# Performance work log

Measured on AMD Instinct MI355X. Metric: run time of the kernel, lower is better.

Reference implementation:

```python
import jax, jax.numpy as jnp
import numpy as np

N_ENT = 40943
N_REL = 237
RANK = 500
BATCH = 1024
NBR = 5
INPUT_SIZE = 600  # neighbor_length(5) * prod(range(1,6)) = 5*120
INIT = 0.001
MIN_NORM = 1e-15
BALL_EPS = 4e-3  # float32 ball projection eps (standard in AttH/GIE repos)


def _artanh(x):
    x = jnp.clip(x, -1.0 + 1e-5, 1.0 - 1e-5)
    return 0.5 * (jnp.log1p(x) - jnp.log1p(-x))


def _project(x, c):
    norm = jnp.maximum(jnp.linalg.norm(x, axis=-1, keepdims=True), MIN_NORM)
    maxnorm = (1.0 - BALL_EPS) / jnp.sqrt(c)
    return jnp.where(norm > maxnorm, x / norm * maxnorm, x)


def _expmap0(u, c):
    sqrt_c = jnp.sqrt(c)
    u_norm = jnp.maximum(jnp.linalg.norm(u, axis=-1, keepdims=True), MIN_NORM)
    gamma = jnp.tanh(sqrt_c * u_norm) * u / (sqrt_c * u_norm)
    return _project(gamma, c)


def _logmap0(y, c):
    sqrt_c = jnp.sqrt(c)
    y_norm = jnp.maximum(jnp.linalg.norm(y, axis=-1, keepdims=True), MIN_NORM)
    return y / y_norm / sqrt_c * _artanh(sqrt_c * y_norm)


def _givens_rotations(r, x):
    b = r.shape[0]
    g = r.reshape(b, -1, 2)
    g = g / jnp.maximum(jnp.linalg.norm(g, axis=-1, keepdims=True), MIN_NORM)
    xr = x.reshape(b, -1, 2)
    x_rot = g[..., 0:1] * xr + g[..., 1:2] * jnp.concatenate([-xr[..., 1:2], xr[..., 0:1]], axis=-1)
    return x_rot.reshape(b, -1)


def setup_inputs() -> dict:
    key = jax.random.key(0)
    ks = jax.random.split(key, 24)
    x = jnp.stack([
        jax.random.randint(ks[0], (BATCH,), 0, N_ENT),
        jax.random.randint(ks[1], (BATCH,), 0, N_REL),
        jax.random.randint(ks[2], (BATCH,), 0, N_ENT),
    ], axis=1)
    neighbors = jnp.concatenate([
        jax.random.randint(ks[3], (N_ENT, NBR, 1), 0, N_ENT),      # neighbor entity ids
        jax.random.randint(ks[4], (N_ENT, NBR, 1), 0, N_REL + 1),  # neighbor rel ids (incl. pad)
    ], axis=2)
    position = jax.random.normal(ks[5], (N_ENT, INPUT_SIZE), jnp.float32)
    lim1 = 1.0 / np.sqrt(INPUT_SIZE)
    lim2 = 1.0 / np.sqrt(RANK)
    limm = 1.0 / np.sqrt(N_REL)
    return {
        'x': x,
        'neighbors': neighbors,
        'position': position,
        'emb_e': INIT * jax.random.normal(ks[6], (N_ENT, 2 * RANK), jnp.float32),
        'emb_r': INIT * jax.random.normal(ks[7], (N_REL + 1, 2 * RANK), jnp.float32),
        'emb1_r': INIT * jax.random.normal(ks[8], (N_REL + 1, 2 * RANK), jnp.float32),
        'context_vec': INIT * jax.random.normal(ks[9], (N_REL, RANK), jnp.float32),
        'neighbor_vec_w': INIT * jax.random.normal(ks[10], (N_REL + 1, RANK), jnp.float32),
        'position_vec_w': INIT * jax.random.normal(ks[11], (N_ENT, INPUT_SIZE), jnp.float32),
        'c1_p': jnp.ones((N_REL, 1), jnp.float32),
        'c2_p': jnp.ones((N_REL, 1), jnp.float32),
        'ab_p': jnp.ones((N_REL + 1, 1), jnp.float32),
        'fc1_w': jax.random.uniform(ks[12], (RANK, INPUT_SIZE), jnp.float32, -lim1, lim1),
        'fc1_b': jax.random.uniform(ks[13], (RANK,), jnp.float32, -lim1, lim1),
        'fc2_w': jax.random.uniform(ks[14], (RANK, RANK), jnp.float32, -lim2, lim2),
        'fc2_b': jax.random.uniform(ks[15], (RANK,), jnp.float32, -lim2, lim2),
        'fc3_w': jax.random.uniform(ks[16], (RANK, RANK), jnp.float32, -lim2, lim2),
        'fc3_b': jax.random.uniform(ks[17], (RANK,), jnp.float32, -lim2, lim2),
        'ln_g': jnp.ones((RANK,), jnp.float32),
        'ln_b': jnp.zeros((RANK,), jnp.float32),
        'fc_mn_w': jax.random.uniform(ks[18], (1, N_REL), jnp.float32, -limm, limm),
        'fc_mn_b': jax.random.uniform(ks[19], (1,), jnp.float32, -limm, limm),
    }


def reference(x, neighbors, position, emb_e, emb_r, emb1_r, context_vec,
              neighbor_vec_w, position_vec_w, c1_p, c2_p, ab_p,
              fc1_w, fc1_b, fc2_w, fc2_b, fc3_w, fc3_b, ln_g, ln_b,
              fc_mn_w, fc_mn_b):
    scale = 1.0 / np.sqrt(RANK)
    h, r = x[:, 0], x[:, 1]
    lhs_full = emb_e[h]                      # (B, 2R)
    rel_full = emb_r[r]                      # (B, 2R)
    rel2 = emb1_r[r][:, :RANK]               # rotation params
    lhs0, lhs1 = lhs_full[:, :RANK], lhs_full[:, RANK:]
    rel0, relb = rel_full[:, :RANK], rel_full[:, RANK:]
    entity1, entity2 = emb_e[:, :RANK], emb_e[:, RANK:]
    # --- neighbor attention (embeddings detached in the original) ---
    nb = neighbors[h]                        # (B, 5, 2)
    ne = jax.lax.stop_gradient(emb_e[nb[:, :, 0]][:, :, :RANK])
    nr = jax.lax.stop_gradient(emb_r[nb[:, :, 1]][:, :, :RANK])
    nv = neighbor_vec_w[nb[:, :, 1]]
    w_n = jax.nn.softmax(jnp.sum(nv * nr * scale, axis=-1, keepdims=True), axis=1)
    att_n = jnp.sum(w_n * ne, axis=1)        # (B, R)
    ab = jnp.mean(jax.nn.softplus(ab_p[nb[:, :, 1]]), axis=1)  # (B, 1)
    # --- positional branch ---
    npos = position[h] * position_vec_w[h] * scale
    npos = npos @ fc1_w.T + fc1_b
    npos = npos @ fc2_w.T + fc2_b
    mu = jnp.mean(npos, axis=-1, keepdims=True)
    var = jnp.var(npos, axis=-1, keepdims=True)
    npos = (npos - mu) / jnp.sqrt(var + 1e-5) * ln_g + ln_b
    npos = npos @ fc3_w.T + fc3_b
    # fc_mn(one_hot) == gather of the relation column of fc_mn_w
    mn_ = jax.nn.softplus(fc_mn_w[:, r].T + fc_mn_b)            # (B, 1)
    lhs = lhs0 + ab * att_n + mn_ * npos
    # --- hyperbolic transforms + 3-candidate attention ---
    c1 = jax.nn.softplus(c1_p[r])
    head1 = _expmap0(lhs, c1)
    res_c1 = _logmap0(_givens_rotations(rel2, head1), c1)
    translation1 = lhs1 * relb
    c2 = jax.nn.softplus(c2_p[r])
    head2 = _expmap0(head1, c2)
    res_c2 = _logmap0(_givens_rotations(rel2, head2), c2)
    translation2 = lhs1 * rel0
    rot_q = _givens_rotations(rel2, head1)
    cands = jnp.stack([res_c1, res_c2, rot_q], axis=1)          # (B, 3, R)
    cv = context_vec[r][:, None, :]
    w_q = jax.nn.softmax(jnp.sum(cv * cands * scale, axis=-1, keepdims=True), axis=1)
    att_q = jnp.sum(w_q * cands, axis=1)                        # (B, R)
    scores = (att_q * rel0 - translation1) @ entity1.T + (att_q * relb + translation2) @ entity2.T
    return scores
```

## Files before the change

kernel.cpp:

```cpp
#include <hip/hip_runtime.h>
#include <math.h>
#include <stdint.h>
#include <stddef.h>

#define N_ENT   40943
#define N_RELC  237
#define RANK    500
#define BATCH   1024
#define NBR     5
#define INSZ    600
#define KPAD    1024
#define SCALE   0.04472135954999579f
#define MINN    1e-15f

typedef __attribute__((ext_vector_type(8))) short  short8;
typedef __attribute__((ext_vector_type(8))) __bf16 bf16x8;
typedef __attribute__((ext_vector_type(4))) float  f32x4;

template <typename V>
static __device__ auto mfma_try(V a, V b, f32x4 c, int)
    -> decltype(__builtin_amdgcn_mfma_f32_16x16x32_bf16(a, b, c, 0, 0, 0)) {
  return __builtin_amdgcn_mfma_f32_16x16x32_bf16(a, b, c, 0, 0, 0);
}
template <typename V>
static __device__ f32x4 mfma_try(V a, V b, f32x4 c, long) {
  bf16x8 ab = __builtin_bit_cast(bf16x8, a);
  bf16x8 bb = __builtin_bit_cast(bf16x8, b);
  return __builtin_amdgcn_mfma_f32_16x16x32_bf16(ab, bb, c, 0, 0, 0);
}
static __device__ inline f32x4 mfma_bf16(short8 a, short8 b, f32x4 c) {
  return mfma_try(a, b, c, 0);
}

static __device__ inline float softplusf(float x) { return log1pf(expf(x)); }
static __device__ inline float artanhf_c(float x) {
  x = fminf(fmaxf(x, -1.0f + 1e-5f), 1.0f - 1e-5f);
  return 0.5f * (log1pf(x) - log1pf(-x));
}
static __device__ inline unsigned short f2bf(float f) {
  union { float f; unsigned int u; } c; c.f = f;
  unsigned int u = c.u;
  return (unsigned short)((u + 0x7FFFu + ((u >> 16) & 1u)) >> 16);
}

__global__ void build_t(const int* __restrict__ x, const float* __restrict__ pos,
                        const float* __restrict__ pvw, float* __restrict__ T) {
  int i = blockIdx.x;
  int h = x[3 * i];
  const float* p = pos + (size_t)h * INSZ;
  const float* w = pvw + (size_t)h * INSZ;
  float* t = T + (size_t)i * INSZ;
  for (int k = threadIdx.x; k < INSZ; k += blockDim.x)
    t[k] = p[k] * w[k] * SCALE;
}

__global__ __launch_bounds__(256) void gemm_fc(
    const float* __restrict__ A, const float* __restrict__ W,
    const float* __restrict__ bias, float* __restrict__ Y,
    int M, int N, int K) {
  __shared__ float As[16][64];
  __shared__ float Bs[16][64];
  int tid = threadIdx.x;
  int tx = tid & 15, ty = tid >> 4;
  int m0 = blockIdx.y * 64, n0 = blockIdx.x * 64;
  float acc[4][4] = {};
  for (int k0 = 0; k0 < K; k0 += 16) {
    int mm = tid & 63, kq = tid >> 6;
    int kk = k0 + kq * 4;
    {
      float v0 = 0, v1 = 0, v2 = 0, v3 = 0;
      int gm = m0 + mm;
      if (gm < M) {
        const float* s = A + (size_t)gm * K + kk;
        if (kk + 3 < K) { float4 v = *(const float4*)s; v0 = v.x; v1 = v.y; v2 = v.z; v3 = v.w; }
        else { if (kk < K) v0 = s[0]; if (kk + 1 < K) v1 = s[1]; if (kk + 2 < K) v2 = s[2]; if (kk + 3 < K) v3 = s[3]; }
      }
      As[kq * 4 + 0][mm] = v0; As[kq * 4 + 1][mm] = v1;
      As[kq * 4 + 2][mm] = v2; As[kq * 4 + 3][mm] = v3;
    }
    {
      float v0 = 0, v1 = 0, v2 = 0, v3 = 0;
      int gn = n0 + mm;
      if (gn < N) {
        const float* s = W + (size_t)gn * K + kk;
        if (kk + 3 < K) { float4 v = *(const float4*)s; v0 = v.x; v1 = v.y; v2 = v.z; v3 = v.w; }
        else { if (kk < K) v0 = s[0]; if (kk + 1 < K) v1 = s[1]; if (kk + 2 < K) v2 = s[2]; if (kk + 3 < K) v3 = s[3]; }
      }
      Bs[kq * 4 + 0][mm] = v0; Bs[kq * 4 + 1][mm] = v1;
      Bs[kq * 4 + 2][mm] = v2; Bs[kq * 4 + 3][mm] = v3;
    }
    __syncthreads();
#pragma unroll
    for (int kk2 = 0; kk2 < 16; kk2++) {
      float a0 = As[kk2][ty * 4 + 0], a1 = As[kk2][ty * 4 + 1];
      float a2 = As[kk2][ty * 4 + 2], a3 = As[kk2][ty * 4 + 3];
      float b0 = Bs[kk2][tx * 4 + 0], b1 = Bs[kk2][tx * 4 + 1];
      float b2 = Bs[kk2][tx * 4 + 2], b3 = Bs[kk2][tx * 4 + 3];
      acc[0][0] += a0 * b0; acc[0][1] += a0 * b1; acc[0][2] += a0 * b2; acc[0][3] += a0 * b3;
      acc[1][0] += a1 * b0; acc[1][1] += a1 * b1; acc[1][2] += a1 * b2; acc[1][3] += a1 * b3;
      acc[2][0] += a2 * b0; acc[2][1] += a2 * b1; acc[2][2] += a2 * b2; acc[2][3] += a2 * b3;
      acc[3][0] += a3 * b0; acc[3][1] += a3 * b1; acc[3][2] += a3 * b2; acc[3][3] += a3 * b3;
    }
    __syncthreads();
  }
#pragma unroll
  for (int i2 = 0; i2 < 4; i2++) {
    int gm = m0 + ty * 4 + i2;
    if (gm >= M) continue;
#pragma unroll
    for (int j = 0; j < 4; j++) {
      int gn = n0 + tx * 4 + j;
      if (gn >= N) continue;
      Y[(size_t)gm * N + gn] = acc[i2][j] + bias[gn];
    }
  }
}

__global__ __launch_bounds__(256) void lnorm(float* __restrict__ Y,
                                             const float* __restrict__ g,
                                             const float* __restrict__ b) {
  __shared__ float s1[256], s2[256];
  int i = blockIdx.x, tid = threadIdx.x;
  float* y = Y + (size_t)i * RANK;
  float x0 = 0, x1 = 0;
  if (tid < RANK) x0 = y[tid];
  if (tid + 256 < RANK) x1 = y[tid + 256];
  s1[tid] = x0 + x1;
  s2[tid] = x0 * x0 + x1 * x1;
  __syncthreads();
  for (int s = 128; s > 0; s >>= 1) {
    if (tid < s) { s1[tid] += s1[tid + s]; s2[tid] += s2[tid + s]; }
    __syncthreads();
  }
  float mu = s1[0] / (float)RANK;
  float var = s2[0] / (float)RANK - mu * mu;
  float rstd = 1.0f / sqrtf(var + 1e-5f);
  if (tid < RANK) y[tid] = (x0 - mu) * rstd * g[tid] + b[tid];
  if (tid + 256 < RANK) y[tid + 256] = (x1 - mu) * rstd * g[tid + 256] + b[tid + 256];
}

static __device__ float block_reduce(float v, float* sred) {
  int tid = threadIdx.x;
  __syncthreads();
  sred[tid] = v;
  __syncthreads();
  for (int s = 128; s > 0; s >>= 1) {
    if (tid < s) sred[tid] += sred[tid + s];
    __syncthreads();
  }
  return sred[0];
}

__global__ __launch_bounds__(256) void rowfinish(
    const int* __restrict__ x, const int* __restrict__ neighbors,
    const float* __restrict__ emb_e, const float* __restrict__ emb_r,
    const float* __restrict__ emb1_r, const float* __restrict__ context_vec,
    const float* __restrict__ nvw, const float* __restrict__ c1_p,
    const float* __restrict__ c2_p, const float* __restrict__ ab_p,
    const float* __restrict__ fc_mn_w, const float* __restrict__ fc_mn_b,
    const float* __restrict__ Y3, unsigned short* __restrict__ Cmat) {
  __shared__ float lhs_s[RANK];
  __shared__ float rot_s[RANK];
  __shared__ float sred[256];
  int i = blockIdx.x, tid = threadIdx.x;
  int h = x[3 * i], r = x[3 * i + 1];
  const float* lhs_full = emb_e + (size_t)h * 1000;
  const float* rel_full = emb_r + (size_t)r * 1000;
  const float* rel2 = emb1_r + (size_t)r * 1000;

  int ne_i[NBR], nr_i[NBR];
#pragma unroll
  for (int j = 0; j < NBR; j++) {
    ne_i[j] = neighbors[h * 10 + 2 * j];
    nr_i[j] = neighbors[h * 10 + 2 * j + 1];
  }
  float pd[NBR];
#pragma unroll
  for (int j = 0; j < NBR; j++) pd[j] = 0.0f;
  for (int k = tid; k < RANK; k += 256) {
#pragma unroll
    for (int j = 0; j < NBR; j++)
      pd[j] += nvw[(size_t)nr_i[j] * RANK + k] * emb_r[(size_t)nr_i[j] * 1000 + k];
  }
  float dnb[NBR];
#pragma unroll
  for (int j = 0; j < NBR; j++) dnb[j] = block_reduce(pd[j], sred) * SCALE;
  float wn[NBR];
  {
    float mx = dnb[0];
#pragma unroll
    for (int j = 1; j < NBR; j++) mx = fmaxf(mx, dnb[j]);
    float s = 0;
#pragma unroll
    for (int j = 0; j < NBR; j++) { wn[j] = expf(dnb[j] - mx); s += wn[j]; }
#pragma unroll
    for (int j = 0; j < NBR; j++) wn[j] /= s;
  }
  float ab = 0;
#pragma unroll
  for (int j = 0; j < NBR; j++) ab += softplusf(ab_p[nr_i[j]]);
  ab *= 0.2f;
  float mn = softplusf(fc_mn_w[r] + fc_mn_b[0]);

  float part = 0;
  for (int k = tid; k < RANK; k += 256) {
    float att = 0;
#pragma unroll
    for (int j = 0; j < NBR; j++) att += wn[j] * emb_e[(size_t)ne_i[j] * 1000 + k];
    float l = lhs_full[k] + ab * att + mn * Y3[(size_t)i * RANK + k];
    lhs_s[k] = l;
    part += l * l;
  }
  float nrm2 = block_reduce(part, sred);
  float norm = fmaxf(sqrtf(nrm2), MINN);
  float c1 = softplusf(c1_p[r]), sc1 = sqrtf(c1);
  float fac = tanhf(sc1 * norm) / (sc1 * norm);
  float gnorm = fac * norm;
  float maxn1 = 0.996f / sc1;
  float a1 = (gnorm > maxn1) ? fac * maxn1 / gnorm : fac;
  float nh1 = fminf(gnorm, maxn1);

  part = 0;
  for (int p = tid; p < RANK / 2; p += 256) {
    float g0 = rel2[2 * p], g1 = rel2[2 * p + 1];
    float gn = fmaxf(sqrtf(g0 * g0 + g1 * g1), MINN);
    g0 /= gn; g1 /= gn;
    float x0 = a1 * lhs_s[2 * p], x1 = a1 * lhs_s[2 * p + 1];
    float r0 = g0 * x0 - g1 * x1;
    float r1 = g0 * x1 + g1 * x0;
    rot_s[2 * p] = r0; rot_s[2 * p + 1] = r1;
    part += r0 * r0 + r1 * r1;
  }
  float yn2 = block_reduce(part, sred);
  float ynorm = fmaxf(sqrtf(yn2), MINN);
  float b1 = artanhf_c(sc1 * ynorm) / (sc1 * ynorm);
  float c2 = softplusf(c2_p[r]), sc2 = sqrtf(c2);
  float fac2 = tanhf(sc2 * nh1) / (sc2 * nh1);
  float g2n = fac2 * nh1, maxn2 = 0.996f / sc2;
  float a2 = (g2n > maxn2) ? fac2 * maxn2 / g2n : fac2;
  float b2 = artanhf_c(sc2 * a2 * ynorm) / (sc2 * ynorm);

  part = 0;
  for (int k = tid; k < RANK; k += 256) part += context_vec[(size_t)r * RANK + k] * rot_s[k];
  float d0 = block_reduce(part, sred) * SCALE;
  float v1 = b1 * d0, v2 = b2 * d0, v3 = d0;
  float mx = fmaxf(v1, fmaxf(v2, v3));
  float e1 = expf(v1 - mx), e2 = expf(v2 - mx), e3 = expf(v3 - mx);
  float gam = (e1 * b1 + e2 * b2 + e3) / (e1 + e2 + e3);

  unsigned short* crow = Cmat + (size_t)i * KPAD;
  for (int k = tid; k < RANK; k += 256) {
    float aq = gam * rot_s[k];
    float r0 = rel_full[k], rb = rel_full[RANK + k], l1 = lhs_full[RANK + k];
    crow[k] = f2bf(aq * r0 - l1 * rb);
    crow[RANK + k] = f2bf(aq * rb + l1 * r0);
  }
  for (int k = 1000 + tid; k < KPAD; k += 256) crow[k] = 0;
}

__global__ __launch_bounds__(256) void convert_b(const float* __restrict__ emb_e,
                                                 unsigned short* __restrict__ Bbf) {
  size_t c = (size_t)blockIdx.x * 256 + threadIdx.x;
  size_t total = (size_t)N_ENT * (KPAD / 8);
  if (c >= total) return;
  int row = (int)(c >> 7);
  int k = (int)(c & 127) * 8;
  unsigned short o[8];
  if (k + 7 < 1000) {
    const float* s = emb_e + (size_t)row * 1000 + k;
#pragma unroll
    for (int j = 0; j < 8; j++) o[j] = f2bf(s[j]);
  } else {
#pragma unroll
    for (int j = 0; j < 8; j++) {
      int kk = k + j;
      o[j] = (kk < 1000) ? f2bf(emb_e[(size_t)row * 1000 + kk]) : (unsigned short)0;
    }
  }
  uint4 v;
  v.x = (unsigned)o[0] | ((unsigned)o[1] << 16);
  v.y = (unsigned)o[2] | ((unsigned)o[3] << 16);
  v.z = (unsigned)o[4] | ((unsigned)o[5] << 16);
  v.w = (unsigned)o[6] | ((unsigned)o[7] << 16);
  *(uint4*)(Bbf + (size_t)row * KPAD + k) = v;
}

template <bool PRECONV>
__global__ __launch_bounds__(256) void gemm_main(
    const unsigned short* __restrict__ Amat, const float* __restrict__ emb_e,
    const unsigned short* __restrict__ Bbf, float* __restrict__ out) {
  __shared__ unsigned short As[128 * 32];
  __shared__ unsigned short Bs[128 * 32];
  int tid = threadIdx.x;
  int m0 = blockIdx.y * 128;
  int n0 = blockIdx.x * 128;
  int lane = tid & 63, wave = tid >> 6;
  int wm = (wave >> 1) * 64, wn = (wave & 1) * 64;
  int quad = lane >> 4, lrow = lane & 15;
  f32x4 acc[4][4];
#pragma unroll
  for (int mi = 0; mi < 4; mi++)
#pragma unroll
    for (int ni = 0; ni < 4; ni++) {
      acc[mi][ni][0] = 0.0f; acc[mi][ni][1] = 0.0f;
      acc[mi][ni][2] = 0.0f; acc[mi][ni][3] = 0.0f;
    }

  for (int k0 = 0; k0 < KPAD; k0 += 32) {
#pragma unroll
    for (int it = 0; it < 2; it++) {
      int c = tid + it * 256;
      int row = c >> 2, kq = c & 3;
      const uint4* src = (const uint4*)(Amat + (size_t)(m0 + row) * KPAD + k0 + kq * 8);
      *(uint4*)(&As[row * 32 + kq * 8]) = *src;
    }
    if (PRECONV) {
#pragma unroll
      for (int it = 0; it < 2; it++) {
        int c = tid + it * 256;
        int row = c >> 2, kq = c & 3;
        int n = n0 + row;
        if (n > N_ENT - 1) n = N_ENT - 1;
        const uint4* src = (const uint4*)(Bbf + (size_t)n * KPAD + k0 + kq * 8);
        *(uint4*)(&Bs[row * 32 + kq * 8]) = *src;
      }
    } else {
#pragma unroll
      for (int it = 0; it < 4; it++) {
        int c = tid + it * 256;
        int row = c >> 3, kq = c & 7;
        int n = n0 + row;
        int kk = k0 + kq * 4;
        float v0 = 0, v1 = 0, v2 = 0, v3 = 0;
        if (n < N_ENT && kk < 1000) {
          float4 v = *(const float4*)(emb_e + (size_t)n * 1000 + kk);
          v0 = v.x; v1 = v.y; v2 = v.z; v3 = v.w;
        }
        uint2 w;
        w.x = (unsigned)f2bf(v0) | ((unsigned)f2bf(v1) << 16);
        w.y = (unsigned)f2bf(v2) | ((unsigned)f2bf(v3) << 16);
        *(uint2*)(&Bs[row * 32 + kq * 4]) = w;
      }
    }
    __syncthreads();
    short8 af[4], bfr[4];
#pragma unroll
    for (int mi = 0; mi < 4; mi++)
      af[mi] = *(const short8*)(&As[(wm + mi * 16 + lrow) * 32 + quad * 8]);
#pragma unroll
    for (int ni = 0; ni < 4; ni++)
      bfr[ni] = *(const short8*)(&Bs[(wn + ni * 16 + lrow) * 32 + quad * 8]);
#pragma unroll
    for (int mi = 0; mi < 4; mi++)
#pragma unroll
      for (int ni = 0; ni < 4; ni++)
        acc[mi][ni] = mfma_bf16(af[mi], bfr[ni], acc[mi][ni]);
    __syncthreads();
  }

#pragma unroll
  for (int mi = 0; mi < 4; mi++) {
#pragma unroll
    for (int ni = 0; ni < 4; ni++) {
      int col = n0 + wn + ni * 16 + lrow;
      if (col >= N_ENT) continue;
      int rowb = m0 + wm + mi * 16 + quad * 4;
#pragma unroll
      for (int i = 0; i < 4; i++)
        out[(size_t)(rowb + i) * N_ENT + col] = acc[mi][ni][i];
    }
  }
}

extern "C" void kernel_launch(void* const* d_in, const int* in_sizes, int n_in,
                              void* d_out, int out_size, void* d_ws, size_t ws_size,
                              hipStream_t stream) {
  const int* x = (const int*)d_in[0];
  const int* neighbors = (const int*)d_in[1];
  const float* position = (const float*)d_in[2];
  const float* emb_e = (const float*)d_in[3];
  const float* emb_r = (const float*)d_in[4];
  const float* emb1_r = (const float*)d_in[5];
  const float* context_vec = (const float*)d_in[6];
  const float* nvw = (const float*)d_in[7];
  const float* pvw = (const float*)d_in[8];
  const float* c1_p = (const float*)d_in[9];
  const float* c2_p = (const float*)d_in[10];
  const float* ab_p = (const float*)d_in[11];
  const float* fc1_w = (const float*)d_in[12];
  const float* fc1_b = (const float*)d_in[13];
  const float* fc2_w = (const float*)d_in[14];
  const float* fc2_b = (const float*)d_in[15];
  const float* fc3_w = (const float*)d_in[16];
  const float* fc3_b = (const float*)d_in[17];
  const float* ln_g = (const float*)d_in[18];
  const float* ln_b = (const float*)d_in[19];
  const float* fc_mn_w = (const float*)d_in[20];
  const float* fc_mn_b = (const float*)d_in[21];
  float* out = (float*)d_out;

  char* ws = (char*)d_ws;
  size_t off = 0;
  auto alloc = [&](size_t bytes) -> void* {
    void* p = (void*)(ws + off);
    off += (bytes + 255) & ~(size_t)255;
    return p;
  };
  float* T = (float*)alloc((size_t)BATCH * INSZ * 4);
  float* Y1 = (float*)alloc((size_t)BATCH * RANK * 4);
  float* Y2 = (float*)alloc((size_t)BATCH * RANK * 4);
  float* Y3 = (float*)alloc((size_t)BATCH * RANK * 4);
  unsigned short* Cmat = (unsigned short*)alloc((size_t)BATCH * KPAD * 2);
  size_t base_need = off;
  size_t bbf_bytes = (size_t)N_ENT * KPAD * 2;
  bool preconv = (ws_size >= base_need + bbf_bytes + 256);
  unsigned short* Bbf = preconv ? (unsigned short*)alloc(bbf_bytes) : nullptr;

  build_t<<<BATCH, 128, 0, stream>>>(x, position, pvw, T);
  gemm_fc<<<dim3(8, 16), 256, 0, stream>>>(T, fc1_w, fc1_b, Y1, BATCH, RANK, INSZ);
  gemm_fc<<<dim3(8, 16), 256, 0, stream>>>(Y1, fc2_w, fc2_b, Y2, BATCH, RANK, RANK);
  lnorm<<<BATCH, 256, 0, stream>>>(Y2, ln_g, ln_b);
  gemm_fc<<<dim3(8, 16), 256, 0, stream>>>(Y2, fc3_w, fc3_b, Y3, BATCH, RANK, RANK);
  rowfinish<<<BATCH, 256, 0, stream>>>(x, neighbors, emb_e, emb_r, emb1_r, context_vec,
                                       nvw, c1_p, c2_p, ab_p, fc_mn_w, fc_mn_b, Y3, Cmat);
  if (preconv) {
    size_t total = (size_t)N_ENT * (KPAD / 8);
    int blocks = (int)((total + 255) / 256);
    convert_b<<<blocks, 256, 0, stream>>>(emb_e, Bbf);
    gemm_main<true><<<dim3(320, 8), 256, 0, stream>>>(Cmat, emb_e, Bbf, out);
  } else {
    gemm_main<false><<<dim3(320, 8), 256, 0, stream>>>(Cmat, emb_e, nullptr, out);
  }
}
```

Measured before the change: 705.0 us.

## Fuse position gather into fc1 GEMM, use direct global-to-LDS loads, swap grid order

Folds the build_t gather-and-scale step into the A-tile load of the first fc GEMM, removing one kernel launch and the T buffer round trip. The main bf16 GEMM now stages A and B tiles with global_load_lds 16-byte loads instead of going through registers. The B buffer is padded to 40960 rows so no row clamping is needed. The grid is transposed so the eight M-blocks that share a B tile run next to each other, improving L2 reuse of the large entity matrix. The risk is that the direct-to-LDS path needs the right waits before the tile is read, and the visible portion does not show how that is handled.

```diff
diff --git a/kernel.cpp b/kernel.cpp
--- a/kernel.cpp
+++ b/kernel.cpp
@@ -4,6 +4,7 @@
 #include <stddef.h>
 
 #define N_ENT   40943
+#define NPAD_B  40960
 #define N_RELC  237
 #define RANK    500
 #define BATCH   1024
@@ -32,6 +33,12 @@
   return mfma_try(a, b, c, 0);
 }
 
+static __device__ inline void gll16(const void* g, void* l) {
+  __builtin_amdgcn_global_load_lds(
+      (const __attribute__((address_space(1))) void*)g,
+      (__attribute__((address_space(3))) void*)l, 16, 0, 0);
+}
+
 static __device__ inline float softplusf(float x) { return log1pf(expf(x)); }
 static __device__ inline float artanhf_c(float x) {
   x = fminf(fmaxf(x, -1.0f + 1e-5f), 1.0f - 1e-5f);
@@ -43,19 +50,11 @@
   return (unsigned short)((u + 0x7FFFu + ((u >> 16) & 1u)) >> 16);
 }
 
-__global__ void build_t(const int* __restrict__ x, const float* __restrict__ pos,
-                        const float* __restrict__ pvw, float* __restrict__ T) {
-  int i = blockIdx.x;
-  int h = x[3 * i];
-  const float* p = pos + (size_t)h * INSZ;
-  const float* w = pvw + (size_t)h * INSZ;
-  float* t = T + (size_t)i * INSZ;
-  for (int k = threadIdx.x; k < INSZ; k += blockDim.x)
-    t[k] = p[k] * w[k] * SCALE;
-}
-
+template <bool FUSE>
 __global__ __launch_bounds__(256) void gemm_fc(
-    const float* __restrict__ A, const float* __restrict__ W,
+    const float* __restrict__ A, const float* __restrict__ A2,
+    const int* __restrict__ xidx,
+    const float* __restrict__ W,
     const float* __restrict__ bias, float* __restrict__ Y,
     int M, int N, int K) {
   __shared__ float As[16][64];
@@ -70,10 +69,17 @@
     {
       float v0 = 0, v1 = 0, v2 = 0, v3 = 0;
       int gm = m0 + mm;
-      if (gm < M) {
-        const float* s = A + (size_t)gm * K + kk;
-        if (kk + 3 < K) { float4 v = *(const float4*)s; v0 = v.x; v1 = v.y; v2 = v.z; v3 = v.w; }
-        else { if (kk < K) v0 = s[0]; if (kk + 1 < K) v1 = s[1]; if (kk + 2 < K) v2 = s[2]; if (kk + 3 < K) v3 = s[3]; }
+      if (gm < M && kk < K) {
+        if (FUSE) {
+          int h = xidx[3 * gm];
+          float4 a = *(const float4*)(A + (size_t)h * K + kk);
+          float4 b = *(const float4*)(A2 + (size_t)h * K + kk);
+          v0 = a.x * b.x * SCALE; v1 = a.y * b.y * SCALE;
+          v2 = a.z * b.z * SCALE; v3 = a.w * b.w * SCALE;
+        } else {
+          float4 v = *(const float4*)(A + (size_t)gm * K + kk);
+          v0 = v.x; v1 = v.y; v2 = v.z; v3 = v.w;
+        }
       }
       As[kq * 4 + 0][mm] = v0; As[kq * 4 + 1][mm] = v1;
       As[kq * 4 + 2][mm] = v2; As[kq * 4 + 3][mm] = v3;
@@ -81,10 +87,9 @@
     {
       float v0 = 0, v1 = 0, v2 = 0, v3 = 0;
       int gn = n0 + mm;
-      if (gn < N) {
-        const float* s = W + (size_t)gn * K + kk;
-        if (kk + 3 < K) { float4 v = *(const float4*)s; v0 = v.x; v1 = v.y; v2 = v.z; v3 = v.w; }
-        else { if (kk < K) v0 = s[0]; if (kk + 1 < K) v1 = s[1]; if (kk + 2 < K) v2 = s[2]; if (kk + 3 < K) v3 = s[3]; }
+      if (gn < N && kk < K) {
+        float4 v = *(const float4*)(W + (size_t)gn * K + kk);
+        v0 = v.x; v1 = v.y; v2 = v.z; v3 = v.w;
       }
       Bs[kq * 4 + 0][mm] = v0; Bs[kq * 4 + 1][mm] = v1;
       Bs[kq * 4 + 2][mm] = v2; Bs[kq * 4 + 3][mm] = v3;
@@ -261,12 +266,12 @@
 __global__ __launch_bounds__(256) void convert_b(const float* __restrict__ emb_e,
                                                  unsigned short* __restrict__ Bbf) {
   size_t c = (size_t)blockIdx.x * 256 + threadIdx.x;
-  size_t total = (size_t)N_ENT * (KPAD / 8);
+  size_t total = (size_t)NPAD_B * (KPAD / 8);
   if (c >= total) return;
   int row = (int)(c >> 7);
   int k = (int)(c & 127) * 8;
   unsigned short o[8];
-  if (k + 7 < 1000) {
+  if (row < N_ENT && k + 7 < 1000) {
     const float* s = emb_e + (size_t)row * 1000 + k;
 #pragma unroll
     for (int j = 0; j < 8; j++) o[j] = f2bf(s[j]);
@@ -274,7 +279,8 @@
 #pragma unroll
     for (int j = 0; j < 8; j++) {
       int kk = k + j;
-      o[j] = (kk < 1000) ? f2bf(emb_e[(size_t)row * 1000 + kk]) : (unsigned short)0;
+      o[j] = (row < N_ENT && kk < 1000) ? f2bf(emb_e[(size_t)row * 1000 + kk])
+                                        : (unsigned short)0;
     }
   }
   uint4 v;
@@ -292,11 +298,12 @@
   __shared__ unsigned short As[128 * 32];
   __shared__ unsigned short Bs[128 * 32];
   int tid = threadIdx.x;
-  int m0 = blockIdx.y * 128;
-  int n0 = blockIdx.x * 128;
+  int m0 = blockIdx.x * 128;
+  int n0 = blockIdx.y * 128;
   int lane = tid & 63, wave = tid >> 6;
   int wm = (wave >> 1) * 64, wn = (wave & 1) * 64;
   int quad = lane >> 4, lrow = lane & 15;
+  int srow = lane >> 2, skq = lane & 3;
   f32x4 acc[4][4];
 #pragma unroll
   for (int mi = 0; mi < 4; mi++)
@@ -309,20 +316,18 @@
   for (int k0 = 0; k0 < KPAD; k0 += 32) {
 #pragma unroll
     for (int it = 0; it < 2; it++) {
-      int c = tid + it * 256;
-      int row = c >> 2, kq = c & 3;
-      const uint4* src = (const uint4*)(Amat + (size_t)(m0 + row) * KPAD + k0 + kq * 8);
-      *(uint4*)(&As[row * 32 + kq * 8]) = *src;
+      int chunk = wave * 2 + it;
+      int row = chunk * 16 + srow;
+      gll16(Amat + (size_t)(m0 + row) * KPAD + k0 + skq * 8,
+            &As[chunk * 512]);
     }
     if (PRECONV) {
 #pragma unroll
       for (int it = 0; it < 2; it++) {
-        int c = tid + it * 256;
-        int row = c >> 2, kq = c & 3;
-        int n = n0 + row;
-        if (n > N_ENT - 1) n = N_ENT - 1;
-        const uint4* src = (const uint4*)(Bbf + (size_t)n * KPAD + k0 + kq * 8);
-        *(uint4*)(&Bs[row * 32 + kq * 8]) = *src;
+        int chunk = wave * 2 + it;
+        int row = chunk * 16 + srow;
+        gll16(Bbf + (size_t)(n0 + row) * KPAD + k0 + skq * 8,
+              &Bs[chunk * 512]);
       }
     } else {
 #pragma unroll
@@ -406,29 +411,30 @@
     off += (bytes + 255) & ~(size_t)255;
     return p;
   };
-  float* T = (float*)alloc((size_t)BATCH * INSZ * 4);
   float* Y1 = (float*)alloc((size_t)BATCH * RANK * 4);
   float* Y2 = (float*)alloc((size_t)BATCH * RANK * 4);
   float* Y3 = (float*)alloc((size_t)BATCH * RANK * 4);
   unsigned short* Cmat = (unsigned short*)alloc((size_t)BATCH * KPAD * 2);
   size_t base_need = off;
-  size_t bbf_bytes = (size_t)N_ENT * KPAD * 2;
+  size_t bbf_bytes = (size_t)NPAD_B * KPAD * 2;
   bool preconv = (ws_size >= base_need + bbf_bytes + 256);
   unsigned short* Bbf = preconv ? (unsigned short*)alloc(bbf_bytes) : nullptr;
 
-  build_t<<<BATCH, 128, 0, stream>>>(x, position, pvw, T);
-  gemm_fc<<<dim3(8, 16), 256, 0, stream>>>(T, fc1_w, fc1_b, Y1, BATCH, RANK, INSZ);
-  gemm_fc<<<dim3(8, 16), 256, 0, stream>>>(Y1, fc2_w, fc2_b, Y2, BATCH, RANK, RANK);
+  gemm_fc<true><<<dim3(8, 16), 256, 0, stream>>>(position, pvw, x, fc1_w, fc1_b, Y1,
+                                                 BATCH, RANK, INSZ);
+  gemm_fc<false><<<dim3(8, 16), 256, 0, stream>>>(Y1, nullptr, nullptr, fc2_w, fc2_b, Y2,
+                                                  BATCH, RANK, RANK);
   lnorm<<<BATCH, 256, 0, stream>>>(Y2, ln_g, ln_b);
-  gemm_fc<<<dim3(8, 16), 256, 0, stream>>>(Y2, fc3_w, fc3_b, Y3, BATCH, RANK, RANK);
+  gemm_fc<false><<<dim3(8, 16), 256, 0, stream>>>(Y2, nullptr, nullptr, fc3_w, fc3_b, Y3,
+                                                  BATCH, RANK, RANK);
   rowfinish<<<BATCH, 256, 0, stream>>>(x, neighbors, emb_e, emb_r, emb1_r, context_vec,
                                        nvw, c1_p, c2_p, ab_p, fc_mn_w, fc_mn_b, Y3, Cmat);
   if (preconv) {
-    size_t total = (size_t)N_ENT * (KPAD / 8);
+    size_t total = (size_t)NPAD_B * (KPAD / 8);
     int blocks = (int)((total + 255) / 256);
     convert_b<<<blocks, 256, 0, stream>>>(emb_e, Bbf);
-    gemm_main<true><<<dim3(320, 8), 256, 0, stream>>>(Cmat, emb_e, Bbf, out);
+    gemm_main<true><<<dim3(8, 320), 256, 0, stream>>>(Cmat, emb_e, Bbf, out);
   } else {
-    gemm_main<false><<<dim3(320, 8), 256, 0, stream>>>(Cmat, emb_e, nullptr, out);
-  }
-}
+    gemm_main<false><<<dim3(8, 320), 256, 0, stream>>>(Cmat, emb_e, nullptr, out);
+  }
+}
```

Measured after the change: 723.9 us. 2.7% more time.
